# Optimization experiments

Measured on AMD Instinct MI355X. Metric: run time of the kernel, lower is better.

The kernel has to match this reference:

```python
import jax, jax.numpy as jnp
import numpy as np

B, N_WAY, N_SHOT, QUERY, NUM_SLOT, D = 64, 5, 5, 15, 8, 640
LAMBDA = 0.1
NEG_INF = jnp.float32(-1e30)


def cover_select(scores):
    # scores: [b, n_way, num_slot]. For each class in order, greedily pick the
    # highest-scoring slot not already taken (replicates torch sort+dedup loop).
    def per_batch(s):
        def step(taken, row):
            sel = jnp.argmax(jnp.where(taken, NEG_INF, row))
            return taken.at[sel].set(True), sel
        _, sel = jax.lax.scan(step, jnp.zeros(s.shape[-1], dtype=bool), s)
        return sel  # [n_way]
    return jax.vmap(per_batch)(scores)  # [b, n_way]


def euclid(gallery, query):
    # gallery [b, n, d], query [b, m, d] -> [b, m, n]
    return jnp.sum((query[:, :, None, :] - gallery[:, None, :, :]) ** 2, axis=-1)


def loss_acc(proto, q, labels_query):
    diff = euclid(proto, q)                                   # [b, n_way*query, n_way]
    logits = jax.nn.log_softmax(-diff, axis=2)
    logits = logits.reshape(B, QUERY, N_WAY, N_WAY)
    nll = -jnp.take_along_axis(logits, labels_query, axis=3).mean()
    y_hat = jnp.argmax(logits, axis=3)
    acc = (y_hat == labels_query[..., 0]).astype(jnp.float32).mean()
    return nll, acc


def setup_inputs() -> dict:
    key = jax.random.key(0)
    k0, k1, k2, k3 = jax.random.split(key, 4)
    n_total = B * N_WAY * (N_SHOT + QUERY)
    out_f = jax.random.normal(k0, (n_total, NUM_SLOT, D), dtype=jnp.float32)
    labels_support = jax.random.randint(k1, (B, N_SHOT, N_WAY, 1), 0, N_WAY, dtype=jnp.int32)
    labels_query = jax.random.randint(k2, (B, QUERY, N_WAY, 1), 0, N_WAY, dtype=jnp.int32)
    att_loss = jax.random.uniform(k3, (1,), dtype=jnp.float32)
    return {"out_f": out_f, "labels_support": labels_support,
            "labels_query": labels_query, "att_loss": att_loss}


def reference(out_f, labels_support, labels_query, att_loss):
    # mode == 'train' path of SimilarityLoss.forward
    b, d = B, out_f.shape[-1]
    ns = b * N_WAY * N_SHOT
    # class prototypes over shots: [b*n_way, num_slot, d]
    sup = out_f[:ns].reshape(b * N_WAY, N_SHOT, NUM_SLOT, d).mean(1)
    qry = out_f[ns:].reshape(b, N_WAY, QUERY, NUM_SLOT, d)

    max_s = cover_select(sup.mean(-1).reshape(b, N_WAY, NUM_SLOT))  # [b, n_way]

    sup_b = sup.reshape(b, N_WAY, NUM_SLOT, d)
    # proto[j, c] = sup_b[j, c, max_s[j, c]]
    proto = jax.vmap(jax.vmap(lambda s, i: s[i]))(sup_b, max_s)     # [b, n_way, d]

    # get_selected path: each class's queries pick that class's selected slot
    out_query = jax.vmap(jax.vmap(lambda q, i: q[:, i, :]))(qry, max_s)  # [b, n_way, query, d]
    out_query = out_query.reshape(b, N_WAY * QUERY, d)

    # get_22 path (faithful to the original non-reset record_temp accumulation):
    # for image s, pick among rows {q22[j, s', max_s[j, i]] : s' <= s, i < n_way}
    # the row with the largest mean over d.
    imgs = N_WAY * QUERY
    q22 = qry.reshape(b, imgs, NUM_SLOT, d)
    cand = jax.vmap(lambda q, i: q[:, i, :])(q22, max_s)            # [b, imgs, n_way, d]
    L = imgs * N_WAY
    m = cand.mean(-1).reshape(b, L)                                 # flat order (s, i)
    prefix = jnp.arange(L)[None, :] < ((jnp.arange(imgs) + 1) * N_WAY)[:, None]  # [imgs, L]
    k = jnp.argmax(jnp.where(prefix[None], m[:, None, :], NEG_INF), axis=-1)     # [b, imgs]
    out_query_t = jnp.take_along_axis(cand.reshape(b, L, d), k[:, :, None], axis=1)  # [b, imgs, d]

    nll, acc = loss_acc(proto, out_query, labels_query)
    loss = nll + jnp.float32(LAMBDA) * att_loss[0]
    loss_t, acc_t = loss_acc(proto, out_query_t, labels_query)
    return (loss, loss_t, acc, acc_t)
```

## Files before the change

### kernel.cpp

```cpp
#include <hip/hip_runtime.h>

#define BB 64
#define N_WAY 5
#define N_SHOT 5
#define QUERY 15
#define NUM_SLOT 8
#define DD 640
#define IMGS (N_WAY * QUERY)
#define NS (BB * N_WAY * N_SHOT)
#define NROWS 6400
#define ROWSZ (NUM_SLOT * DD)
#define F4_PER_SLOT 160
#define NELEM (BB * IMGS)
#define NGROUP (BB * N_WAY)
#define BPB 4
#define EPB 19
#define NBATCHBLK (BB * BPB)

__global__ __launch_bounds__(256) void k_pass1(const float* __restrict__ out_f,
                                               float* __restrict__ rowmean,
                                               float* __restrict__ proto_all,
                                               float* __restrict__ pn2_all) {
    int b = blockIdx.x;
    int t = threadIdx.x;
    int slot = t >> 5;
    int l = t & 31;
    if (b < NGROUP) {
        const int g = b;
        float4 acc[5];
        #pragma unroll
        for (int k = 0; k < 5; ++k) acc[k] = make_float4(0.f, 0.f, 0.f, 0.f);
        #pragma unroll
        for (int sh = 0; sh < N_SHOT; ++sh) {
            const float4* p = (const float4*)(out_f +
                ((size_t)((g * N_SHOT + sh) * NUM_SLOT + slot)) * DD);
            float s = 0.f;
            #pragma unroll
            for (int k = 0; k < 5; ++k) {
                float4 v = p[l + k * 32];
                acc[k].x += v.x; acc[k].y += v.y; acc[k].z += v.z; acc[k].w += v.w;
                s += (v.x + v.y) + (v.z + v.w);
            }
            #pragma unroll
            for (int off = 16; off; off >>= 1) s += __shfl_down(s, off, 32);
            if (l == 0) rowmean[(g * N_SHOT + sh) * NUM_SLOT + slot] = s * (1.f / DD);
        }
        float4* pp = (float4*)(proto_all + ((size_t)(g * NUM_SLOT + slot)) * DD);
        float ssq = 0.f;
        #pragma unroll
        for (int k = 0; k < 5; ++k) {
            acc[k].x *= 0.2f; acc[k].y *= 0.2f; acc[k].z *= 0.2f; acc[k].w *= 0.2f;
            pp[l + k * 32] = acc[k];
            ssq += acc[k].x * acc[k].x + acc[k].y * acc[k].y
                 + acc[k].z * acc[k].z + acc[k].w * acc[k].w;
        }
        #pragma unroll
        for (int off = 16; off; off >>= 1) ssq += __shfl_down(ssq, off, 32);
        if (l == 0) pn2_all[g * NUM_SLOT + slot] = ssq;
    } else {
        int r = NS + (b - NGROUP);
        const float4* p = (const float4*)(out_f + (size_t)r * ROWSZ) + slot * F4_PER_SLOT;
        float s = 0.f;
        #pragma unroll
        for (int k = 0; k < 5; ++k) {
            float4 v = p[l + k * 32];
            s += (v.x + v.y) + (v.z + v.w);
        }
        #pragma unroll
        for (int off = 16; off; off >>= 1) s += __shfl_down(s, off, 32);
        if (l == 0) rowmean[r * NUM_SLOT + slot] = s * (1.f / DD);
    }
}

__global__ __launch_bounds__(256) void k_batch(const float* __restrict__ out_f,
                                               const float* __restrict__ rowmean,
                                               const float* __restrict__ proto_all,
                                               const float* __restrict__ pn2_all,
                                               const int* __restrict__ labels_query,
                                               float* __restrict__ part) {
    int blk = blockIdx.x;
    int j = blk >> 2;
    int piece = blk & 3;
    int t = threadIdx.x;
    int wave = t >> 6, lane = t & 63;

    __shared__ float qb[IMGS * NUM_SLOT];
    __shared__ float supm[N_WAY * NUM_SLOT];
    __shared__ int   msS[N_WAY];
    __shared__ float protoS[N_WAY * DD];
    __shared__ float pn2S[N_WAY];
    __shared__ int   kS[IMGS];
    __shared__ float partial[4][4];

    const float* qbase = rowmean + (size_t)(NS + j * IMGS) * NUM_SLOT;
    for (int i = t; i < IMGS * NUM_SLOT; i += 256) qb[i] = qbase[i];
    if (t < N_WAY * NUM_SLOT) {
        int c = t >> 3, s = t & 7;
        const float* sb = rowmean + (size_t)j * (N_WAY * N_SHOT * NUM_SLOT)
                          + c * (N_SHOT * NUM_SLOT) + s;
        supm[t] = (sb[0] + sb[8] + sb[16] + sb[24] + sb[32]) * 0.2f;
    }
    __syncthreads();

    if (t == 0) {
        unsigned taken = 0u;
        #pragma unroll
        for (int c = 0; c < N_WAY; ++c) {
            float best = -3.0e38f; int bi = 0;
            #pragma unroll
            for (int s = 0; s < NUM_SLOT; ++s) {
                float v = supm[c * NUM_SLOT + s];
                if (!((taken >> s) & 1u) && v > best) { best = v; bi = s; }
            }
            taken |= (1u << bi);
            msS[c] = bi;
        }
    }
    __syncthreads();

    if (wave == 0) {
        int ms0 = msS[0], ms1 = msS[1], ms2 = msS[2], ms3 = msS[3], ms4 = msS[4];
        float bv; int bi;
        {
            const float* q = &qb[lane * NUM_SLOT];
            bv = q[ms0]; bi = lane * N_WAY;
            float v;
            v = q[ms1]; if (v > bv) { bv = v; bi = lane * N_WAY + 1; }
            v = q[ms2]; if (v > bv) { bv = v; bi = lane * N_WAY + 2; }
            v = q[ms3]; if (v > bv) { bv = v; bi = lane * N_WAY + 3; }
            v = q[ms4]; if (v > bv) { bv = v; bi = lane * N_WAY + 4; }
        }
        #pragma unroll
        for (int off = 1; off < 64; off <<= 1) {
            float ov = __shfl_up(bv, off, 64);
            int   oi = __shfl_up(bi, off, 64);
            if (lane >= off && !(bv > ov)) { bv = ov; bi = oi; }
        }
        kS[lane] = bi;
        float tv = __shfl(bv, 63, 64);
        int   ti = __shfl(bi, 63, 64);
        float bv2 = -3.0e38f; int bi2 = 0;
        if (lane < IMGS - 64) {
            int s = 64 + lane;
            const float* q = &qb[s * NUM_SLOT];
            bv2 = q[ms0]; bi2 = s * N_WAY;
            float v;
            v = q[ms1]; if (v > bv2) { bv2 = v; bi2 = s * N_WAY + 1; }
            v = q[ms2]; if (v > bv2) { bv2 = v; bi2 = s * N_WAY + 2; }
            v = q[ms3]; if (v > bv2) { bv2 = v; bi2 = s * N_WAY + 3; }
            v = q[ms4]; if (v > bv2) { bv2 = v; bi2 = s * N_WAY + 4; }
        }
        #pragma unroll
        for (int off = 1; off < 16; off <<= 1) {
            float ov = __shfl_up(bv2, off, 64);
            int   oi = __shfl_up(bi2, off, 64);
            if (lane >= off && lane < IMGS - 64 && !(bv2 > ov)) { bv2 = ov; bi2 = oi; }
        }
        if (lane < IMGS - 64) {
            if (!(bv2 > tv)) { bv2 = tv; bi2 = ti; }
            kS[64 + lane] = bi2;
        }
    } else {
        int idx = t - 64;
        for (int i = idx; i < N_WAY * F4_PER_SLOT; i += 192) {
            int c = i / F4_PER_SLOT, r = i - c * F4_PER_SLOT;
            int g = j * N_WAY + c;
            ((float4*)protoS)[i] =
                ((const float4*)(proto_all + ((size_t)(g * NUM_SLOT + msS[c])) * DD))[r];
        }
        if (idx < N_WAY) pn2S[idx] = pn2_all[(j * N_WAY + idx) * NUM_SLOT + msS[idx]];
    }
    __syncthreads();

    int e_lo = piece * EPB;
    int e_hi = (piece + 1) * EPB; if (e_hi > IMGS) e_hi = IMGS;
    float lnll1 = 0.f, lnll2 = 0.f, lacc1 = 0.f, lacc2 = 0.f;
    for (int m = e_lo + wave; m < e_hi; m += 4) {
        int bid = j * IMGS + m;
        int ms1 = msS[m / QUERY];
        const float4* q1 = (const float4*)(out_f + (size_t)(NS + bid) * ROWSZ + ms1 * DD);
        int kk = kS[m];
        int s2 = kk / N_WAY, c2 = kk - s2 * N_WAY;
        int ms2 = msS[c2];
        const float4* q2 = (const float4*)(out_f +
            (size_t)(NS + j * IMGS + s2) * ROWSZ + ms2 * DD);

        float s1[N_WAY] = {0, 0, 0, 0, 0};
        float s2a[N_WAY] = {0, 0, 0, 0, 0};
        for (int i = lane; i < F4_PER_SLOT; i += 64) {
            float4 a = q1[i];
            float4 bq = q2[i];
            #pragma unroll
            for (int n = 0; n < N_WAY; ++n) {
                float4 p = ((const float4*)protoS)[n * F4_PER_SLOT + i];
                s1[n]  += a.x * p.x + a.y * p.y + a.z * p.z + a.w * p.w;
                s2a[n] += bq.x * p.x + bq.y * p.y + bq.z * p.z + bq.w * p.w;
            }
        }
        #pragma unroll
        for (int n = 0; n < N_WAY; ++n) {
            #pragma unroll
            for (int off = 32; off; off >>= 1) {
                s1[n]  += __shfl_down(s1[n],  off, 64);
                s2a[n] += __shfl_down(s2a[n], off, 64);
            }
        }
        if (lane == 0) {
            int label = labels_query[bid];
            {
                float li[N_WAY]; float mx = -3.0e38f;
                #pragma unroll
                for (int n = 0; n < N_WAY; ++n) { li[n] = 2.f * s1[n] - pn2S[n]; mx = fmaxf(mx, li[n]); }
                float se = 0.f;
                #pragma unroll
                for (int n = 0; n < N_WAY; ++n) se += expf(li[n] - mx);
                float lse = mx + logf(se);
                int bi = 0; float bvv = li[0];
                #pragma unroll
                for (int n = 1; n < N_WAY; ++n) if (li[n] > bvv) { bvv = li[n]; bi = n; }
                lnll1 += -(li[label] - lse);
                lacc1 += (bi == label) ? 1.f : 0.f;
            }
            {
                float li[N_WAY]; float mx = -3.0e38f;
                #pragma unroll
                for (int n = 0; n < N_WAY; ++n) { li[n] = 2.f * s2a[n] - pn2S[n]; mx = fmaxf(mx, li[n]); }
                float se = 0.f;
                #pragma unroll
                for (int n = 0; n < N_WAY; ++n) se += expf(li[n] - mx);
                float lse = mx + logf(se);
                int bi = 0; float bvv = li[0];
                #pragma unroll
                for (int n = 1; n < N_WAY; ++n) if (li[n] > bvv) { bvv = li[n]; bi = n; }
                lnll2 += -(li[label] - lse);
                lacc2 += (bi == label) ? 1.f : 0.f;
            }
        }
    }
    if (lane == 0) {
        partial[wave][0] = lnll1;
        partial[wave][1] = lnll2;
        partial[wave][2] = lacc1;
        partial[wave][3] = lacc2;
    }
    __syncthreads();
    if (t == 0) {
        #pragma unroll
        for (int c = 0; c < 4; ++c)
            part[c * NBATCHBLK + blk] =
                partial[0][c] + partial[1][c] + partial[2][c] + partial[3][c];
    }
}

__global__ __launch_bounds__(256) void k_final(const float* __restrict__ part,
                                               const float* __restrict__ att_loss,
                                               float* __restrict__ out) {
    __shared__ float red[256];
    int t = threadIdx.x;
    for (int c = 0; c < 4; ++c) {
        red[t] = part[c * NBATCHBLK + t];
        __syncthreads();
        for (int w = 128; w; w >>= 1) {
            if (t < w) red[t] += red[t + w];
            __syncthreads();
        }
        if (t == 0) {
            float v = red[0] / (float)NELEM;
            if (c == 0) v += 0.1f * att_loss[0];
            out[c] = v;
        }
        __syncthreads();
    }
}

extern "C" void kernel_launch(void* const* d_in, const int* in_sizes, int n_in,
                              void* d_out, int out_size, void* d_ws, size_t ws_size,
                              hipStream_t stream) {
    const float* out_f        = (const float*)d_in[0];
    const int*   labels_query = (const int*)d_in[2];
    const float* att_loss     = (const float*)d_in[3];
    float* out = (float*)d_out;

    float* rowmean   = (float*)d_ws;
    float* proto_all = rowmean + NROWS * NUM_SLOT;
    float* pn2_all   = proto_all + NGROUP * NUM_SLOT * DD;
    float* part      = pn2_all + NGROUP * NUM_SLOT;

    k_pass1<<<NGROUP + NELEM, 256, 0, stream>>>(out_f, rowmean, proto_all, pn2_all);
    k_batch<<<NBATCHBLK, 256, 0, stream>>>(out_f, rowmean, proto_all, pn2_all,
                                           labels_query, part);
    k_final<<<1, 256, 0, stream>>>(part, att_loss, out);
}
```

Measured before the change: 47.38 us.

## Launch one block per query element instead of four blocks per batch

Replaces the per-batch k_batch kernel (256 blocks, waves looping over about 19 elements each) with k_elem, which launches one block per query element (4800 blocks). Each block recomputes the cover selection and a prefix argmax up to its own image. It then reads prototypes straight from global memory instead of staging them in LDS, and reduces the dot products across waves through shared memory. Per-element results are written as float4 and summed in a single pass in k_final. The goal is more parallelism and better latency hiding on the second kernel, at the cost of redundant per-block setup work and repeated prototype reads through cache.

Result: slower. 52.82 us (+11.5%).

```diff
diff --git a/kernel.cpp b/kernel.cpp
--- a/kernel.cpp
+++ b/kernel.cpp
@@ -13,9 +13,6 @@
 #define F4_PER_SLOT 160
 #define NELEM (BB * IMGS)
 #define NGROUP (BB * N_WAY)
-#define BPB 4
-#define EPB 19
-#define NBATCHBLK (BB * BPB)
 
 __global__ __launch_bounds__(256) void k_pass1(const float* __restrict__ out_f,
                                                float* __restrict__ rowmean,
@@ -72,33 +69,32 @@
     }
 }
 
-__global__ __launch_bounds__(256) void k_batch(const float* __restrict__ out_f,
-                                               const float* __restrict__ rowmean,
-                                               const float* __restrict__ proto_all,
-                                               const float* __restrict__ pn2_all,
-                                               const int* __restrict__ labels_query,
-                                               float* __restrict__ part) {
-    int blk = blockIdx.x;
-    int j = blk >> 2;
-    int piece = blk & 3;
+__global__ __launch_bounds__(256) void k_elem(const float* __restrict__ out_f,
+                                              const float* __restrict__ rowmean,
+                                              const float* __restrict__ proto_all,
+                                              const float* __restrict__ pn2_all,
+                                              const int* __restrict__ labels_query,
+                                              float4* __restrict__ part) {
+    int bid = blockIdx.x;
+    int j = bid / IMGS, m = bid - j * IMGS;
     int t = threadIdx.x;
     int wave = t >> 6, lane = t & 63;
 
-    __shared__ float qb[IMGS * NUM_SLOT];
+    __shared__ __align__(16) float qb[IMGS * NUM_SLOT];
     __shared__ float supm[N_WAY * NUM_SLOT];
     __shared__ int   msS[N_WAY];
-    __shared__ float protoS[N_WAY * DD];
-    __shared__ float pn2S[N_WAY];
-    __shared__ int   kS[IMGS];
-    __shared__ float partial[4][4];
+    __shared__ int   kkS;
+    __shared__ float p2S[N_WAY];
+    __shared__ float red[4][10];
 
     const float* qbase = rowmean + (size_t)(NS + j * IMGS) * NUM_SLOT;
-    for (int i = t; i < IMGS * NUM_SLOT; i += 256) qb[i] = qbase[i];
-    if (t < N_WAY * NUM_SLOT) {
-        int c = t >> 3, s = t & 7;
+    if (t < 150) ((float4*)qb)[t] = ((const float4*)qbase)[t];
+    if (t >= 192 && t < 192 + N_WAY * NUM_SLOT) {
+        int idx = t - 192;
+        int c = idx >> 3, s = idx & 7;
         const float* sb = rowmean + (size_t)j * (N_WAY * N_SHOT * NUM_SLOT)
                           + c * (N_SHOT * NUM_SLOT) + s;
-        supm[t] = (sb[0] + sb[8] + sb[16] + sb[24] + sb[32]) * 0.2f;
+        supm[idx] = (sb[0] + sb[8] + sb[16] + sb[24] + sb[32]) * 0.2f;
     }
     __syncthreads();
 
@@ -118,158 +114,132 @@
     }
     __syncthreads();
 
+    if (t < N_WAY) p2S[t] = pn2_all[(j * N_WAY + t) * NUM_SLOT + msS[t]];
+
     if (wave == 0) {
-        int ms0 = msS[0], ms1 = msS[1], ms2 = msS[2], ms3 = msS[3], ms4 = msS[4];
-        float bv; int bi;
-        {
-            const float* q = &qb[lane * NUM_SLOT];
-            bv = q[ms0]; bi = lane * N_WAY;
-            float v;
-            v = q[ms1]; if (v > bv) { bv = v; bi = lane * N_WAY + 1; }
-            v = q[ms2]; if (v > bv) { bv = v; bi = lane * N_WAY + 2; }
-            v = q[ms3]; if (v > bv) { bv = v; bi = lane * N_WAY + 3; }
-            v = q[ms4]; if (v > bv) { bv = v; bi = lane * N_WAY + 4; }
-        }
-        #pragma unroll
-        for (int off = 1; off < 64; off <<= 1) {
-            float ov = __shfl_up(bv, off, 64);
-            int   oi = __shfl_up(bi, off, 64);
-            if (lane >= off && !(bv > ov)) { bv = ov; bi = oi; }
-        }
-        kS[lane] = bi;
-        float tv = __shfl(bv, 63, 64);
-        int   ti = __shfl(bi, 63, 64);
-        float bv2 = -3.0e38f; int bi2 = 0;
-        if (lane < IMGS - 64) {
-            int s = 64 + lane;
-            const float* q = &qb[s * NUM_SLOT];
-            bv2 = q[ms0]; bi2 = s * N_WAY;
-            float v;
-            v = q[ms1]; if (v > bv2) { bv2 = v; bi2 = s * N_WAY + 1; }
-            v = q[ms2]; if (v > bv2) { bv2 = v; bi2 = s * N_WAY + 2; }
-            v = q[ms3]; if (v > bv2) { bv2 = v; bi2 = s * N_WAY + 3; }
-            v = q[ms4]; if (v > bv2) { bv2 = v; bi2 = s * N_WAY + 4; }
-        }
-        #pragma unroll
-        for (int off = 1; off < 16; off <<= 1) {
-            float ov = __shfl_up(bv2, off, 64);
-            int   oi = __shfl_up(bi2, off, 64);
-            if (lane >= off && lane < IMGS - 64 && !(bv2 > ov)) { bv2 = ov; bi2 = oi; }
-        }
-        if (lane < IMGS - 64) {
-            if (!(bv2 > tv)) { bv2 = tv; bi2 = ti; }
-            kS[64 + lane] = bi2;
-        }
-    } else {
-        int idx = t - 64;
-        for (int i = idx; i < N_WAY * F4_PER_SLOT; i += 192) {
-            int c = i / F4_PER_SLOT, r = i - c * F4_PER_SLOT;
-            int g = j * N_WAY + c;
-            ((float4*)protoS)[i] =
-                ((const float4*)(proto_all + ((size_t)(g * NUM_SLOT + msS[c])) * DD))[r];
-        }
-        if (idx < N_WAY) pn2S[idx] = pn2_all[(j * N_WAY + idx) * NUM_SLOT + msS[idx]];
-    }
-    __syncthreads();
-
-    int e_lo = piece * EPB;
-    int e_hi = (piece + 1) * EPB; if (e_hi > IMGS) e_hi = IMGS;
-    float lnll1 = 0.f, lnll2 = 0.f, lacc1 = 0.f, lacc2 = 0.f;
-    for (int m = e_lo + wave; m < e_hi; m += 4) {
-        int bid = j * IMGS + m;
-        int ms1 = msS[m / QUERY];
+        float v = -3.0e38f; int idx = 0x7fffffff;
+        #pragma unroll
+        for (int rep = 0; rep < 2; ++rep) {
+            int s = lane + rep * 64;
+            if (s <= m) {
+                const float* q = &qb[s * NUM_SLOT];
+                #pragma unroll
+                for (int c = 0; c < N_WAY; ++c) {
+                    float x = q[msS[c]];
+                    if (x > v) { v = x; idx = s * N_WAY + c; }
+                }
+            }
+        }
+        #pragma unroll
+        for (int off = 32; off; off >>= 1) {
+            float ov = __shfl_down(v, off, 64);
+            int   oi = __shfl_down(idx, off, 64);
+            if (ov > v || (ov == v && oi < idx)) { v = ov; idx = oi; }
+        }
+        if (lane == 0) kkS = idx;
+    }
+    __syncthreads();
+
+    int ms1 = msS[m / QUERY];
+    int kk = kkS;
+    int s2 = kk / N_WAY, c2 = kk - s2 * N_WAY;
+    int ms2 = msS[c2];
+
+    float s1[N_WAY] = {0, 0, 0, 0, 0};
+    float s2a[N_WAY] = {0, 0, 0, 0, 0};
+    if (t < F4_PER_SLOT) {
         const float4* q1 = (const float4*)(out_f + (size_t)(NS + bid) * ROWSZ + ms1 * DD);
-        int kk = kS[m];
-        int s2 = kk / N_WAY, c2 = kk - s2 * N_WAY;
-        int ms2 = msS[c2];
         const float4* q2 = (const float4*)(out_f +
             (size_t)(NS + j * IMGS + s2) * ROWSZ + ms2 * DD);
-
-        float s1[N_WAY] = {0, 0, 0, 0, 0};
-        float s2a[N_WAY] = {0, 0, 0, 0, 0};
-        for (int i = lane; i < F4_PER_SLOT; i += 64) {
-            float4 a = q1[i];
-            float4 bq = q2[i];
+        float4 a = q1[t];
+        float4 bq = q2[t];
+        #pragma unroll
+        for (int n = 0; n < N_WAY; ++n) {
+            const float4* pr = (const float4*)(proto_all +
+                ((size_t)((j * N_WAY + n) * NUM_SLOT + msS[n])) * DD);
+            float4 p = pr[t];
+            s1[n]  += a.x * p.x + a.y * p.y + a.z * p.z + a.w * p.w;
+            s2a[n] += bq.x * p.x + bq.y * p.y + bq.z * p.z + bq.w * p.w;
+        }
+    }
+    #pragma unroll
+    for (int n = 0; n < N_WAY; ++n) {
+        #pragma unroll
+        for (int off = 32; off; off >>= 1) {
+            s1[n]  += __shfl_down(s1[n],  off, 64);
+            s2a[n] += __shfl_down(s2a[n], off, 64);
+        }
+    }
+    if (lane == 0) {
+        #pragma unroll
+        for (int n = 0; n < N_WAY; ++n) { red[wave][n] = s1[n]; red[wave][5 + n] = s2a[n]; }
+    }
+    __syncthreads();
+    if (t == 0) {
+        int label = labels_query[bid];
+        float nll1, nll2, acc1, acc2;
+        {
+            float li[N_WAY]; float mx = -3.0e38f;
             #pragma unroll
             for (int n = 0; n < N_WAY; ++n) {
-                float4 p = ((const float4*)protoS)[n * F4_PER_SLOT + i];
-                s1[n]  += a.x * p.x + a.y * p.y + a.z * p.z + a.w * p.w;
-                s2a[n] += bq.x * p.x + bq.y * p.y + bq.z * p.z + bq.w * p.w;
-            }
-        }
-        #pragma unroll
-        for (int n = 0; n < N_WAY; ++n) {
-            #pragma unroll
-            for (int off = 32; off; off >>= 1) {
-                s1[n]  += __shfl_down(s1[n],  off, 64);
-                s2a[n] += __shfl_down(s2a[n], off, 64);
-            }
-        }
-        if (lane == 0) {
-            int label = labels_query[bid];
-            {
-                float li[N_WAY]; float mx = -3.0e38f;
-                #pragma unroll
-                for (int n = 0; n < N_WAY; ++n) { li[n] = 2.f * s1[n] - pn2S[n]; mx = fmaxf(mx, li[n]); }
-                float se = 0.f;
-                #pragma unroll
-                for (int n = 0; n < N_WAY; ++n) se += expf(li[n] - mx);
-                float lse = mx + logf(se);
-                int bi = 0; float bvv = li[0];
-                #pragma unroll
-                for (int n = 1; n < N_WAY; ++n) if (li[n] > bvv) { bvv = li[n]; bi = n; }
-                lnll1 += -(li[label] - lse);
-                lacc1 += (bi == label) ? 1.f : 0.f;
-            }
-            {
-                float li[N_WAY]; float mx = -3.0e38f;
-                #pragma unroll
-                for (int n = 0; n < N_WAY; ++n) { li[n] = 2.f * s2a[n] - pn2S[n]; mx = fmaxf(mx, li[n]); }
-                float se = 0.f;
-                #pragma unroll
-                for (int n = 0; n < N_WAY; ++n) se += expf(li[n] - mx);
-                float lse = mx + logf(se);
-                int bi = 0; float bvv = li[0];
-                #pragma unroll
-                for (int n = 1; n < N_WAY; ++n) if (li[n] > bvv) { bvv = li[n]; bi = n; }
-                lnll2 += -(li[label] - lse);
-                lacc2 += (bi == label) ? 1.f : 0.f;
-            }
-        }
-    }
-    if (lane == 0) {
-        partial[wave][0] = lnll1;
-        partial[wave][1] = lnll2;
-        partial[wave][2] = lacc1;
-        partial[wave][3] = lacc2;
-    }
-    __syncthreads();
-    if (t == 0) {
-        #pragma unroll
-        for (int c = 0; c < 4; ++c)
-            part[c * NBATCHBLK + blk] =
-                partial[0][c] + partial[1][c] + partial[2][c] + partial[3][c];
-    }
-}
-
-__global__ __launch_bounds__(256) void k_final(const float* __restrict__ part,
+                float sc = red[0][n] + red[1][n] + red[2][n] + red[3][n];
+                li[n] = 2.f * sc - p2S[n]; mx = fmaxf(mx, li[n]);
+            }
+            float se = 0.f;
+            #pragma unroll
+            for (int n = 0; n < N_WAY; ++n) se += expf(li[n] - mx);
+            float lse = mx + logf(se);
+            int bi = 0; float bvv = li[0];
+            #pragma unroll
+            for (int n = 1; n < N_WAY; ++n) if (li[n] > bvv) { bvv = li[n]; bi = n; }
+            nll1 = -(li[label] - lse);
+            acc1 = (bi == label) ? 1.f : 0.f;
+        }
+        {
+            float li[N_WAY]; float mx = -3.0e38f;
+            #pragma unroll
+            for (int n = 0; n < N_WAY; ++n) {
+                float sc = red[0][5 + n] + red[1][5 + n] + red[2][5 + n] + red[3][5 + n];
+                li[n] = 2.f * sc - p2S[n]; mx = fmaxf(mx, li[n]);
+            }
+            float se = 0.f;
+            #pragma unroll
+            for (int n = 0; n < N_WAY; ++n) se += expf(li[n] - mx);
+            float lse = mx + logf(se);
+            int bi = 0; float bvv = li[0];
+            #pragma unroll
+            for (int n = 1; n < N_WAY; ++n) if (li[n] > bvv) { bvv = li[n]; bi = n; }
+            nll2 = -(li[label] - lse);
+            acc2 = (bi == label) ? 1.f : 0.f;
+        }
+        part[bid] = make_float4(nll1, nll2, acc1, acc2);
+    }
+}
+
+__global__ __launch_bounds__(256) void k_final(const float4* __restrict__ part,
                                                const float* __restrict__ att_loss,
                                                float* __restrict__ out) {
-    __shared__ float red[256];
+    __shared__ float4 red[256];
     int t = threadIdx.x;
-    for (int c = 0; c < 4; ++c) {
-        red[t] = part[c * NBATCHBLK + t];
+    float4 s = make_float4(0.f, 0.f, 0.f, 0.f);
+    for (int i = t; i < NELEM; i += 256) {
+        float4 v = part[i];
+        s.x += v.x; s.y += v.y; s.z += v.z; s.w += v.w;
+    }
+    red[t] = s;
+    __syncthreads();
+    for (int w = 128; w; w >>= 1) {
+        if (t < w) {
+            red[t].x += red[t + w].x; red[t].y += red[t + w].y;
+            red[t].z += red[t + w].z; red[t].w += red[t + w].w;
+        }
         __syncthreads();
-        for (int w = 128; w; w >>= 1) {
-            if (t < w) red[t] += red[t + w];
-            __syncthreads();
-        }
-        if (t == 0) {
-            float v = red[0] / (float)NELEM;
-            if (c == 0) v += 0.1f * att_loss[0];
-            out[c] = v;
-        }
-        __syncthreads();
+    }
+    if (t == 0) {
+        out[0] = red[0].x / (float)NELEM + 0.1f * att_loss[0];
+        out[1] = red[0].y / (float)NELEM;
+        out[2] = red[0].z / (float)NELEM;
+        out[3] = red[0].w / (float)NELEM;
     }
 }
 
@@ -281,13 +251,13 @@
     const float* att_loss     = (const float*)d_in[3];
     float* out = (float*)d_out;
 
-    float* rowmean   = (float*)d_ws;
-    float* proto_all = rowmean + NROWS * NUM_SLOT;
-    float* pn2_all   = proto_all + NGROUP * NUM_SLOT * DD;
-    float* part      = pn2_all + NGROUP * NUM_SLOT;
+    float*  rowmean   = (float*)d_ws;
+    float*  proto_all = rowmean + NROWS * NUM_SLOT;
+    float*  pn2_all   = proto_all + NGROUP * NUM_SLOT * DD;
+    float4* part      = (float4*)(pn2_all + NGROUP * NUM_SLOT);
 
     k_pass1<<<NGROUP + NELEM, 256, 0, stream>>>(out_f, rowmean, proto_all, pn2_all);
-    k_batch<<<NBATCHBLK, 256, 0, stream>>>(out_f, rowmean, proto_all, pn2_all,
-                                           labels_query, part);
+    k_elem<<<NELEM, 256, 0, stream>>>(out_f, rowmean, proto_all, pn2_all,
+                                      labels_query, part);
     k_final<<<1, 256, 0, stream>>>(part, att_loss, out);
 }
```
